# Kernel tuning notes

Hardware: AMD Instinct MI355X
Metric: run time of the kernel (lower is better)

## Reference

```python
import jax, jax.numpy as jnp
import numpy as np

B, S, D, H = 64, 2048, 512, 512


def setup_inputs() -> dict:
    key = jax.random.key(0)
    ks = jax.random.split(key, 8)
    return {
        "hidden": jax.random.normal(ks[0], (B, D), dtype=jnp.float32),
        "context": jax.random.normal(ks[1], (B, S, D), dtype=jnp.float32),
        "mask": jax.random.randint(ks[2], (B, S), 0, 2).astype(bool),
        "Wd": jax.random.normal(ks[3], (H, D), dtype=jnp.float32) * 0.05,
        "bd": jax.random.normal(ks[4], (H,), dtype=jnp.float32) * 0.05,
        "We": jax.random.normal(ks[5], (H, D), dtype=jnp.float32) * 0.05,
        "be": jax.random.normal(ks[6], (H,), dtype=jnp.float32) * 0.05,
        "V": jax.random.normal(ks[7], (H,), dtype=jnp.float32) * 0.05,
    }


def reference(hidden, context, mask, Wd, bd, We, be, V):
    # di = d_linear(hidden): [B, H]
    di = hidden @ Wd.T + bd
    # ei = e_linear(context): [B, S, H]
    ei = jnp.einsum("bsd,hd->bsh", context, We) + be
    # additive score u_i = V . tanh(di + ei): [B, S]
    ui = jnp.einsum("h,bsh->bs", V, jnp.tanh(di[:, None, :] + ei))
    # masked positions get -inf (ui[mask] = -inf)
    ui = jnp.where(mask, -jnp.inf, ui)
    alpha = jax.nn.softmax(ui, axis=-1)  # [B, S]
    # context aggregation uses the PROJECTED context ei (as in torch code)
    attention_hidden_state = jnp.einsum("bsh,bs->bh", ei, alpha)
    return alpha, attention_hidden_state
```

## Files before the change

### kernel.cpp

```cpp
#include <hip/hip_runtime.h>
#include <cstdint>

#define B_ 64
#define S_ 2048
#define D_ 512
#define H_ 512

using f32x4  = __attribute__((ext_vector_type(4))) float;
using bf16x8 = __attribute__((ext_vector_type(8))) short;

__device__ __forceinline__ unsigned short f2bf(float f) {
  unsigned u = __float_as_uint(f);
  u += 0x7FFFu + ((u >> 16) & 1u);
  return (unsigned short)(u >> 16);
}
__device__ __forceinline__ float bf2f(unsigned short h) {
  return __uint_as_float(((unsigned)h) << 16);
}
__device__ __forceinline__ float fast_tanh(float x) {
  float t = __builtin_amdgcn_exp2f(x * 2.8853900817779268f);
  return 1.0f - 2.0f * __builtin_amdgcn_rcpf(t + 1.0f);
}

__device__ __forceinline__ void gl_lds16(const unsigned short* g, unsigned short* l) {
  __builtin_amdgcn_global_load_lds(
      (const __attribute__((address_space(1))) unsigned int*)g,
      (__attribute__((address_space(3))) unsigned int*)l, 16, 0, 0);
}

__global__ void k_cvt(const float* __restrict__ src, unsigned short* __restrict__ dst, int n8) {
  int i = blockIdx.x * 256 + threadIdx.x;
  if (i >= n8) return;
  const f32x4* p = (const f32x4*)(src + (size_t)i * 8);
  f32x4 a = p[0], b = p[1];
  bf16x8 o;
  o[0] = (short)f2bf(a[0]); o[1] = (short)f2bf(a[1]);
  o[2] = (short)f2bf(a[2]); o[3] = (short)f2bf(a[3]);
  o[4] = (short)f2bf(b[0]); o[5] = (short)f2bf(b[1]);
  o[6] = (short)f2bf(b[2]); o[7] = (short)f2bf(b[3]);
  *(bf16x8*)(dst + (size_t)i * 8) = o;
}

__global__ void k_di(const float* __restrict__ hidden, const float* __restrict__ Wd,
                     const float* __restrict__ bd, float* __restrict__ di) {
  int idx = blockIdx.x * 256 + threadIdx.x;
  int h = idx >> 6;
  int b = idx & 63;
  const f32x4* hp = (const f32x4*)(hidden + (size_t)b * D_);
  const f32x4* wp = (const f32x4*)(Wd + (size_t)h * D_);
  float acc = 0.f;
#pragma unroll 8
  for (int i = 0; i < D_ / 4; ++i) {
    f32x4 x = hp[i], y = wp[i];
    acc += x[0] * y[0] + x[1] * y[1] + x[2] * y[2] + x[3] * y[3];
  }
  di[b * H_ + h] = acc + bd[h];
}

__global__ __launch_bounds__(256, 4) void k_ei_gemm(
    const unsigned short* __restrict__ A, const unsigned short* __restrict__ Bw,
    const float* __restrict__ be, const float* __restrict__ V,
    const float* __restrict__ di, float* __restrict__ ui4) {
  __shared__ __align__(16) unsigned short ldsA[2][128 * 32];
  __shared__ __align__(16) unsigned short ldsB[2][128 * 32];
  __shared__ float ured[4][64];

  const int bid = blockIdx.x;
  const int swz = (bid & 7) * 512 + (bid >> 3);
  const int row0 = (swz >> 2) << 7;
  const int nt   = swz & 3;
  const int col0 = nt << 7;

  const int t  = threadIdx.x;
  const int l  = t & 63;
  const int w  = t >> 6;
  const int wm = (w >> 1) << 6;
  const int wn = (w & 1) << 6;
  const int lr = l & 15;
  const int lg = l >> 4;

  const int sr = l >> 2;
  const int sc = ((l & 3) ^ ((sr >> 1) & 3)) << 3;
  const unsigned short* gA = A + (size_t)(row0 + w * 32 + sr) * D_ + sc;
  const unsigned short* gB = Bw + (size_t)(col0 + w * 32 + sr) * D_ + sc;
  unsigned short* lA[2] = {&ldsA[0][w * 1024], &ldsA[1][w * 1024]};
  unsigned short* lB[2] = {&ldsB[0][w * 1024], &ldsB[1][w * 1024]};

  const int rslot = (lg ^ ((lr >> 1) & 3)) << 3;

#define STAGE(bf, kk) do {                      \
    const int k0_ = (kk) << 5;                  \
    gl_lds16(gA + k0_,           lA[bf]);       \
    gl_lds16(gA + 16 * D_ + k0_, lA[bf] + 512); \
    gl_lds16(gB + k0_,           lB[bf]);       \
    gl_lds16(gB + 16 * D_ + k0_, lB[bf] + 512); \
  } while (0)

  f32x4 acc[4][4];
  const f32x4 z = {0.f, 0.f, 0.f, 0.f};
#pragma unroll
  for (int mi = 0; mi < 4; ++mi)
#pragma unroll
    for (int ni = 0; ni < 4; ++ni) acc[mi][ni] = z;

  STAGE(0, 0);
  int cur = 0;
  for (int kt = 0; kt < 16; ++kt) {
    __syncthreads();
    if (kt < 15) STAGE(cur ^ 1, kt + 1);

    bf16x8 af[4], bq[4];
#pragma unroll
    for (int mi = 0; mi < 4; ++mi)
      af[mi] = *(const bf16x8*)&ldsA[cur][(wm + mi * 16 + lr) * 32 + rslot];
#pragma unroll
    for (int ni = 0; ni < 4; ++ni)
      bq[ni] = *(const bf16x8*)&ldsB[cur][(wn + ni * 16 + lr) * 32 + rslot];
#pragma unroll
    for (int mi = 0; mi < 4; ++mi)
#pragma unroll
      for (int ni = 0; ni < 4; ++ni)
        acc[mi][ni] = __builtin_amdgcn_mfma_f32_16x16x32_bf16(
            af[mi], bq[ni], acc[mi][ni], 0, 0, 0);
    cur ^= 1;
  }
#undef STAGE

  const int b = row0 >> 11;
  float uacc[4][4];
#pragma unroll
  for (int mi = 0; mi < 4; ++mi)
#pragma unroll
    for (int j = 0; j < 4; ++j) uacc[mi][j] = 0.f;

#pragma unroll
  for (int ni = 0; ni < 4; ++ni) {
    const int gc = col0 + wn + ni * 16 + lr;
    const float vv = V[gc];
    const float base = di[b * H_ + gc] + be[gc];
#pragma unroll
    for (int mi = 0; mi < 4; ++mi)
#pragma unroll
      for (int j = 0; j < 4; ++j)
        uacc[mi][j] += vv * fast_tanh(base + acc[mi][ni][j]);
  }
#pragma unroll
  for (int mi = 0; mi < 4; ++mi)
#pragma unroll
    for (int j = 0; j < 4; ++j) {
      float s = uacc[mi][j];
      s += __shfl_xor(s, 1);
      s += __shfl_xor(s, 2);
      s += __shfl_xor(s, 4);
      s += __shfl_xor(s, 8);
      if (lr == 0) ured[w][mi * 16 + (lg << 2) + j] = s;
    }
  __syncthreads();
  if (t < 128) {
    const int r = t & 63, half = t >> 6;
    const float v = ured[half * 2][r] + ured[half * 2 + 1][r];
    ui4[nt * (B_ * S_) + row0 + half * 64 + r] = v;
  }
}

__global__ void k_softmax(const float* __restrict__ ui4, const void* __restrict__ mask,
                          float* __restrict__ alpha) {
  __shared__ float red[4];
  __shared__ int sfl;
  const int b = blockIdx.x, t = threadIdx.x;
  const int l = t & 63, w = t >> 6;

  if (t == 0) sfl = 0;
  const unsigned int* mw = (const unsigned int*)mask;
  unsigned det = (mw[b * 512 + t] | mw[b * 512 + 256 + t]) & 0xFFFFFF00u;
  __syncthreads();
  if (det) atomicOr(&sfl, 1);
  __syncthreads();
  const int fl = sfl;

  float u[8];
#pragma unroll
  for (int i = 0; i < 8; ++i) {
    const int idx = b * S_ + t + i * 256;
    const int msk = fl ? (int)((const unsigned char*)mask)[idx]
                       : ((const int*)mask)[idx];
    const float uv = ui4[idx] + ui4[idx + B_ * S_] + ui4[idx + 2 * B_ * S_] +
                     ui4[idx + 3 * B_ * S_];
    u[i] = msk ? -__builtin_inff() : uv;
  }

  float mx = u[0];
#pragma unroll
  for (int i = 1; i < 8; ++i) mx = fmaxf(mx, u[i]);
#pragma unroll
  for (int off = 32; off; off >>= 1) mx = fmaxf(mx, __shfl_xor(mx, off));
  if (l == 0) red[w] = mx;
  __syncthreads();
  mx = fmaxf(fmaxf(red[0], red[1]), fmaxf(red[2], red[3]));
  __syncthreads();

  float p[8];
  float s = 0.f;
#pragma unroll
  for (int i = 0; i < 8; ++i) {
    p[i] = __builtin_amdgcn_exp2f((u[i] - mx) * 1.4426950408889634f);
    s += p[i];
  }
#pragma unroll
  for (int off = 32; off; off >>= 1) s += __shfl_xor(s, off);
  if (l == 0) red[w] = s;
  __syncthreads();
  s = red[0] + red[1] + red[2] + red[3];

  const float inv = 1.0f / s;
#pragma unroll
  for (int i = 0; i < 8; ++i) alpha[b * S_ + t + i * 256] = p[i] * inv;
}

__global__ void k_wsum(const unsigned short* __restrict__ ctxb, const float* __restrict__ alpha,
                       float* __restrict__ part) {
  __shared__ float red[3][512];
  const int b = blockIdx.x >> 4, chunk = blockIdx.x & 15;
  const int t = threadIdx.x;
  const int h0 = (t & 63) << 3;
  const int sw = t >> 6;
  const int s0 = chunk << 7;

  float acc[8] = {0.f, 0.f, 0.f, 0.f, 0.f, 0.f, 0.f, 0.f};
#pragma unroll 4
  for (int k = 0; k < 32; ++k) {
    const int s = s0 + sw + (k << 2);
    const float a = alpha[b * S_ + s];
    bf16x8 e = *(const bf16x8*)(ctxb + ((size_t)(b * S_ + s)) * D_ + h0);
#pragma unroll
    for (int j = 0; j < 8; ++j) acc[j] += a * bf2f((unsigned short)e[j]);
  }
  if (sw) {
#pragma unroll
    for (int j = 0; j < 8; ++j) red[sw - 1][h0 + j] = acc[j];
  }
  __syncthreads();
  if (sw == 0) {
#pragma unroll
    for (int j = 0; j < 8; ++j)
      part[((chunk << 6) + b) * 512 + h0 + j] =
          acc[j] + red[0][h0 + j] + red[1][h0 + j] + red[2][h0 + j];
  }
}

__global__ void k_collapse(const float* __restrict__ part, float* __restrict__ wsum) {
  const int i = blockIdx.x * 256 + threadIdx.x;
  const int b = i >> 9, d = i & 511;
  float s = 0.f;
#pragma unroll
  for (int c = 0; c < 16; ++c) s += part[((c << 6) + b) * 512 + d];
  wsum[i] = s;
}

__global__ void k_out1(const float* __restrict__ wsum, const float* __restrict__ We,
                       const float* __restrict__ be, float* __restrict__ out1) {
  int idx = blockIdx.x * 256 + threadIdx.x;
  int h = idx >> 6;
  int b = idx & 63;
  const f32x4* wp = (const f32x4*)(wsum + (size_t)b * D_);
  const f32x4* ep = (const f32x4*)(We + (size_t)h * D_);
  float acc = 0.f;
#pragma unroll 8
  for (int i = 0; i < D_ / 4; ++i) {
    f32x4 x = wp[i], y = ep[i];
    acc += x[0] * y[0] + x[1] * y[1] + x[2] * y[2] + x[3] * y[3];
  }
  out1[b * H_ + h] = acc + be[h];
}

extern "C" void kernel_launch(void* const* d_in, const int* in_sizes, int n_in,
                              void* d_out, int out_size, void* d_ws, size_t ws_size,
                              hipStream_t stream) {
  const float* hidden = (const float*)d_in[0];
  const float* ctx    = (const float*)d_in[1];
  const void*  mask   = d_in[2];
  const float* Wd     = (const float*)d_in[3];
  const float* bd     = (const float*)d_in[4];
  const float* We     = (const float*)d_in[5];
  const float* be     = (const float*)d_in[6];
  const float* V      = (const float*)d_in[7];

  float* out   = (float*)d_out;
  float* alpha = out;
  float* out1  = out + B_ * S_;

  char* ws = (char*)d_ws;
  const size_t off_ctxb = 0;
  const size_t off_u2   = off_ctxb + (size_t)B_ * S_ * D_ * 2;
  const size_t off_r3   = off_u2 + 4ull * B_ * S_ * 4;
  const size_t off_web  = off_r3 + (size_t)B_ * H_ * 4;

  unsigned short* ctxb = (unsigned short*)(ws + off_ctxb);
  float* ui4  = (float*)(ws + off_u2);
  float* part = (float*)(ws + off_u2);
  float* di   = (float*)(ws + off_r3);
  float* wsum = (float*)(ws + off_r3);
  unsigned short* Web = (unsigned short*)(ws + off_web);

  k_cvt<<<(B_ * S_ * D_ / 8) / 256, 256, 0, stream>>>(ctx, ctxb, B_ * S_ * D_ / 8);
  k_cvt<<<(H_ * D_ / 8) / 256, 256, 0, stream>>>(We, Web, H_ * D_ / 8);
  k_di<<<(B_ * H_) / 256, 256, 0, stream>>>(hidden, Wd, bd, di);
  k_ei_gemm<<<(B_ * S_ / 128) * 4, 256, 0, stream>>>(ctxb, Web, be, V, di, ui4);
  k_softmax<<<B_, 256, 0, stream>>>(ui4, mask, alpha);
  k_wsum<<<B_ * 16, 256, 0, stream>>>(ctxb, alpha, part);
  k_collapse<<<(B_ * D_) / 256, 256, 0, stream>>>(part, wsum);
  k_out1<<<(B_ * H_) / 256, 256, 0, stream>>>(wsum, We, be, out1);
}
```

Baseline: 246.8 us.

## Enlarge ei GEMM tile to 256x128 with 8 waves and explicit vmcnt pipelining

The ei GEMM block now covers 256 rows by 128 columns using 512 threads (8 waves), so each B tile loaded into LDS is reused across twice as many rows. The main loop preloads two stages up front and replaces __syncthreads with raw s_barrier plus explicit vmcnt waits, so direct-to-LDS loads can stay in flight across iterations. It also raises wave priority around the MFMA block. The hand-written vmcnt counts and raw barriers depend on exact load ordering and could give races if the compiler emits other memory ops, and the larger block raises LDS use per block, which may reduce occupancy.

```diff
diff --git a/kernel.cpp b/kernel.cpp
--- a/kernel.cpp
+++ b/kernel.cpp
@@ -26,6 +26,12 @@
   __builtin_amdgcn_global_load_lds(
       (const __attribute__((address_space(1))) unsigned int*)g,
       (__attribute__((address_space(3))) unsigned int*)l, 16, 0, 0);
+}
+
+__device__ __forceinline__ void barrier_raw() {
+  asm volatile("" ::: "memory");
+  __builtin_amdgcn_s_barrier();
+  asm volatile("" ::: "memory");
 }
 
 __global__ void k_cvt(const float* __restrict__ src, unsigned short* __restrict__ dst, int n8) {
@@ -57,17 +63,17 @@
   di[b * H_ + h] = acc + bd[h];
 }
 
-__global__ __launch_bounds__(256, 4) void k_ei_gemm(
+__global__ __launch_bounds__(512, 4) void k_ei_gemm(
     const unsigned short* __restrict__ A, const unsigned short* __restrict__ Bw,
     const float* __restrict__ be, const float* __restrict__ V,
     const float* __restrict__ di, float* __restrict__ ui4) {
-  __shared__ __align__(16) unsigned short ldsA[2][128 * 32];
+  __shared__ __align__(16) unsigned short ldsA[2][256 * 32];
   __shared__ __align__(16) unsigned short ldsB[2][128 * 32];
-  __shared__ float ured[4][64];
+  __shared__ float ured[8][64];
 
   const int bid = blockIdx.x;
-  const int swz = (bid & 7) * 512 + (bid >> 3);
-  const int row0 = (swz >> 2) << 7;
+  const int swz = (bid & 7) * 256 + (bid >> 3);
+  const int row0 = (swz >> 2) << 8;
   const int nt   = swz & 3;
   const int col0 = nt << 7;
 
@@ -80,20 +86,17 @@
   const int lg = l >> 4;
 
   const int sr = l >> 2;
-  const int sc = ((l & 3) ^ ((sr >> 1) & 3)) << 3;
-  const unsigned short* gA = A + (size_t)(row0 + w * 32 + sr) * D_ + sc;
-  const unsigned short* gB = Bw + (size_t)(col0 + w * 32 + sr) * D_ + sc;
-  unsigned short* lA[2] = {&ldsA[0][w * 1024], &ldsA[1][w * 1024]};
-  unsigned short* lB[2] = {&ldsB[0][w * 1024], &ldsB[1][w * 1024]};
+  const int sc = ((l & 3) ^ ((l >> 3) & 3)) << 3;
+  const unsigned short* gA = A + (size_t)(row0 + w * 16 + sr) * D_ + sc;
+  const unsigned short* gB = Bw + (size_t)(col0 + w * 16 + sr) * D_ + sc;
 
   const int rslot = (lg ^ ((lr >> 1) & 3)) << 3;
 
-#define STAGE(bf, kk) do {                      \
-    const int k0_ = (kk) << 5;                  \
-    gl_lds16(gA + k0_,           lA[bf]);       \
-    gl_lds16(gA + 16 * D_ + k0_, lA[bf] + 512); \
-    gl_lds16(gB + k0_,           lB[bf]);       \
-    gl_lds16(gB + 16 * D_ + k0_, lB[bf] + 512); \
+#define STAGE(bf, kk) do {                                          \
+    const int k0_ = (kk) << 5;                                      \
+    gl_lds16(gA + k0_,            &ldsA[bf][w * 512]);              \
+    gl_lds16(gA + 128 * D_ + k0_, &ldsA[bf][4096 + w * 512]);       \
+    gl_lds16(gB + k0_,            &ldsB[bf][w * 512]);              \
   } while (0)
 
   f32x4 acc[4][4];
@@ -104,25 +107,35 @@
     for (int ni = 0; ni < 4; ++ni) acc[mi][ni] = z;
 
   STAGE(0, 0);
-  int cur = 0;
+  STAGE(1, 1);
+
   for (int kt = 0; kt < 16; ++kt) {
-    __syncthreads();
-    if (kt < 15) STAGE(cur ^ 1, kt + 1);
-
+    if (kt < 15)
+      asm volatile("s_waitcnt vmcnt(3)" ::: "memory");
+    else
+      asm volatile("s_waitcnt vmcnt(0)" ::: "memory");
+    barrier_raw();
+
+    const int bf = kt & 1;
     bf16x8 af[4], bq[4];
 #pragma unroll
     for (int mi = 0; mi < 4; ++mi)
-      af[mi] = *(const bf16x8*)&ldsA[cur][(wm + mi * 16 + lr) * 32 + rslot];
+      af[mi] = *(const bf16x8*)&ldsA[bf][(wm + mi * 16 + lr) * 32 + rslot];
 #pragma unroll
     for (int ni = 0; ni < 4; ++ni)
-      bq[ni] = *(const bf16x8*)&ldsB[cur][(wn + ni * 16 + lr) * 32 + rslot];
+      bq[ni] = *(const bf16x8*)&ldsB[bf][(wn + ni * 16 + lr) * 32 + rslot];
+
+    __builtin_amdgcn_s_setprio(1);
 #pragma unroll
     for (int mi = 0; mi < 4; ++mi)
 #pragma unroll
       for (int ni = 0; ni < 4; ++ni)
         acc[mi][ni] = __builtin_amdgcn_mfma_f32_16x16x32_bf16(
             af[mi], bq[ni], acc[mi][ni], 0, 0, 0);
-    cur ^= 1;
+    __builtin_amdgcn_s_setprio(0);
+
+    barrier_raw();
+    if (kt + 2 < 16) STAGE(bf, kt + 2);
   }
 #undef STAGE
 
@@ -156,10 +169,9 @@
       if (lr == 0) ured[w][mi * 16 + (lg << 2) + j] = s;
     }
   __syncthreads();
-  if (t < 128) {
-    const int r = t & 63, half = t >> 6;
-    const float v = ured[half * 2][r] + ured[half * 2 + 1][r];
-    ui4[nt * (B_ * S_) + row0 + half * 64 + r] = v;
+  if (t < 256) {
+    const int band = t >> 6, r = t & 63;
+    ui4[nt * (B_ * S_) + row0 + t] = ured[band * 2][r] + ured[band * 2 + 1][r];
   }
 }
 
@@ -305,7 +317,7 @@
   k_cvt<<<(B_ * S_ * D_ / 8) / 256, 256, 0, stream>>>(ctx, ctxb, B_ * S_ * D_ / 8);
   k_cvt<<<(H_ * D_ / 8) / 256, 256, 0, stream>>>(We, Web, H_ * D_ / 8);
   k_di<<<(B_ * H_) / 256, 256, 0, stream>>>(hidden, Wd, bd, di);
-  k_ei_gemm<<<(B_ * S_ / 128) * 4, 256, 0, stream>>>(ctxb, Web, be, V, di, ui4);
+  k_ei_gemm<<<(B_ * S_ / 256) * 4, 512, 0, stream>>>(ctxb, Web, be, V, di, ui4);
   k_softmax<<<B_, 256, 0, stream>>>(ui4, mask, alpha);
   k_wsum<<<B_ * 16, 256, 0, stream>>>(ctxb, alpha, part);
   k_collapse<<<(B_ * D_) / 256, 256, 0, stream>>>(part, wsum);
```

Result: faster. 239.0 us (-3.2%).

## Fuse bf16 context conversion into GEMM register staging and merge small kernels

Applied to the files above, without the earlier changes.

The separate full-context fp32-to-bf16 conversion pass is removed. The GEMM now loads fp32 context tiles into registers, converts them with packed cvt instructions and writes them to swizzled LDS, using register-prefetch double buffering, raw barriers and setprio around the MFMA block. The di and We-conversion kernels are merged into one prep launch, and collapse plus out1 are merged into one tail kernel. k_wsum now reads fp32 context directly, which doubles that kernel's read traffic but avoids writing and rereading a bf16 copy; occupancy bounds drop from 4 to 3.

```diff
diff --git a/kernel.cpp b/kernel.cpp
--- a/kernel.cpp
+++ b/kernel.cpp
@@ -8,57 +8,60 @@
 
 using f32x4  = __attribute__((ext_vector_type(4))) float;
 using bf16x8 = __attribute__((ext_vector_type(8))) short;
+using u32x2  = __attribute__((ext_vector_type(2))) unsigned int;
 
 __device__ __forceinline__ unsigned short f2bf(float f) {
   unsigned u = __float_as_uint(f);
   u += 0x7FFFu + ((u >> 16) & 1u);
   return (unsigned short)(u >> 16);
 }
-__device__ __forceinline__ float bf2f(unsigned short h) {
-  return __uint_as_float(((unsigned)h) << 16);
+__device__ __forceinline__ unsigned int cvtpk(float lo, float hi) {
+  unsigned int r;
+  asm("v_cvt_pk_bf16_f32 %0, %1, %2" : "=v"(r) : "v"(lo), "v"(hi));
+  return r;
 }
 __device__ __forceinline__ float fast_tanh(float x) {
   float t = __builtin_amdgcn_exp2f(x * 2.8853900817779268f);
   return 1.0f - 2.0f * __builtin_amdgcn_rcpf(t + 1.0f);
 }
 
-__device__ __forceinline__ void gl_lds16(const unsigned short* g, unsigned short* l) {
-  __builtin_amdgcn_global_load_lds(
-      (const __attribute__((address_space(1))) unsigned int*)g,
-      (__attribute__((address_space(3))) unsigned int*)l, 16, 0, 0);
-}
-
-__global__ void k_cvt(const float* __restrict__ src, unsigned short* __restrict__ dst, int n8) {
-  int i = blockIdx.x * 256 + threadIdx.x;
-  if (i >= n8) return;
-  const f32x4* p = (const f32x4*)(src + (size_t)i * 8);
-  f32x4 a = p[0], b = p[1];
-  bf16x8 o;
-  o[0] = (short)f2bf(a[0]); o[1] = (short)f2bf(a[1]);
-  o[2] = (short)f2bf(a[2]); o[3] = (short)f2bf(a[3]);
-  o[4] = (short)f2bf(b[0]); o[5] = (short)f2bf(b[1]);
-  o[6] = (short)f2bf(b[2]); o[7] = (short)f2bf(b[3]);
-  *(bf16x8*)(dst + (size_t)i * 8) = o;
-}
-
-__global__ void k_di(const float* __restrict__ hidden, const float* __restrict__ Wd,
-                     const float* __restrict__ bd, float* __restrict__ di) {
-  int idx = blockIdx.x * 256 + threadIdx.x;
-  int h = idx >> 6;
-  int b = idx & 63;
-  const f32x4* hp = (const f32x4*)(hidden + (size_t)b * D_);
-  const f32x4* wp = (const f32x4*)(Wd + (size_t)h * D_);
-  float acc = 0.f;
+__device__ __forceinline__ void barrier_raw() {
+  asm volatile("" ::: "memory");
+  __builtin_amdgcn_s_barrier();
+  asm volatile("" ::: "memory");
+}
+
+__global__ void k_prep(const float* __restrict__ hidden, const float* __restrict__ Wd,
+                       const float* __restrict__ bd, float* __restrict__ di,
+                       const float* __restrict__ We, unsigned short* __restrict__ Web) {
+  if (blockIdx.x < 128) {
+    int idx = blockIdx.x * 256 + threadIdx.x;
+    int h = idx >> 6;
+    int b = idx & 63;
+    const f32x4* hp = (const f32x4*)(hidden + (size_t)b * D_);
+    const f32x4* wp = (const f32x4*)(Wd + (size_t)h * D_);
+    float acc = 0.f;
 #pragma unroll 8
-  for (int i = 0; i < D_ / 4; ++i) {
-    f32x4 x = hp[i], y = wp[i];
-    acc += x[0] * y[0] + x[1] * y[1] + x[2] * y[2] + x[3] * y[3];
-  }
-  di[b * H_ + h] = acc + bd[h];
-}
-
-__global__ __launch_bounds__(256, 4) void k_ei_gemm(
-    const unsigned short* __restrict__ A, const unsigned short* __restrict__ Bw,
+    for (int i = 0; i < D_ / 4; ++i) {
+      f32x4 x = hp[i], y = wp[i];
+      acc += x[0] * y[0] + x[1] * y[1] + x[2] * y[2] + x[3] * y[3];
+    }
+    di[b * H_ + h] = acc + bd[h];
+  } else {
+    int i = (blockIdx.x - 128) * 256 + threadIdx.x;
+    const f32x4* p = (const f32x4*)(We + (size_t)i * 8);
+    f32x4 a = p[0], b = p[1];
+    bf16x8 o;
+    o[0] = (short)f2bf(a[0]); o[1] = (short)f2bf(a[1]);
+    o[2] = (short)f2bf(a[2]); o[3] = (short)f2bf(a[3]);
+    o[4] = (short)f2bf(b[0]); o[5] = (short)f2bf(b[1]);
+    o[6] = (short)f2bf(b[2]); o[7] = (short)f2bf(b[3]);
+    *(bf16x8*)(Web + (size_t)i * 8) = o;
+  }
+}
+
+__global__ __launch_bounds__(256, 3) void k_ei_gemm(
+    const float* __restrict__ A, const unsigned short* __restrict__ Bw,
     const float* __restrict__ be, const float* __restrict__ V,
     const float* __restrict__ di, float* __restrict__ ui4) {
   __shared__ __align__(16) unsigned short ldsA[2][128 * 32];
@@ -79,21 +82,41 @@
   const int lr = l & 15;
   const int lg = l >> 4;
 
-  const int sr = l >> 2;
-  const int sc = ((l & 3) ^ ((sr >> 1) & 3)) << 3;
-  const unsigned short* gA = A + (size_t)(row0 + w * 32 + sr) * D_ + sc;
-  const unsigned short* gB = Bw + (size_t)(col0 + w * 32 + sr) * D_ + sc;
-  unsigned short* lA[2] = {&ldsA[0][w * 1024], &ldsA[1][w * 1024]};
-  unsigned short* lB[2] = {&ldsB[0][w * 1024], &ldsB[1][w * 1024]};
-
-  const int rslot = (lg ^ ((lr >> 1) & 3)) << 3;
-
-#define STAGE(bf, kk) do {                      \
-    const int k0_ = (kk) << 5;                  \
-    gl_lds16(gA + k0_,           lA[bf]);       \
-    gl_lds16(gA + 16 * D_ + k0_, lA[bf] + 512); \
-    gl_lds16(gB + k0_,           lB[bf]);       \
-    gl_lds16(gB + 16 * D_ + k0_, lB[bf] + 512); \
+  const float* gA = A + (size_t)(row0 + w * 32 + (l >> 3)) * D_ + ((l & 7) << 2);
+  const unsigned short* gB = Bw + (size_t)(col0 + w * 32 + (l >> 2)) * D_ + ((l & 3) << 3);
+
+  const int sA = (((l & 7) >> 1) ^ ((l >> 4) & 3));
+  const int eA0 = (w * 32 + (l >> 3)) * 32 + sA * 8 + (l & 1) * 4;
+  const int sB = ((l & 3) ^ ((l >> 3) & 3));
+  const int eB0 = (w * 32 + (l >> 2)) * 32 + sB * 8;
+
+  const int rs = (lg ^ ((lr >> 1) & 3)) << 3;
+
+  f32x4  rA0, rA1, rA2, rA3;
+  bf16x8 rB0, rB1;
+
+#define LOAD(kk) do {                                   \
+    const float* a_ = gA + ((kk) << 5);                 \
+    rA0 = *(const f32x4*)(a_);                          \
+    rA1 = *(const f32x4*)(a_ + 8 * D_);                 \
+    rA2 = *(const f32x4*)(a_ + 16 * D_);                \
+    rA3 = *(const f32x4*)(a_ + 24 * D_);                \
+    const unsigned short* b_ = gB + ((kk) << 5);        \
+    rB0 = *(const bf16x8*)(b_);                         \
+    rB1 = *(const bf16x8*)(b_ + 16 * D_);               \
+  } while (0)
+
+#define WRITE(bf) do {                                                  \
+    u32x2 p0 = {cvtpk(rA0[0], rA0[1]), cvtpk(rA0[2], rA0[3])};          \
+    u32x2 p1 = {cvtpk(rA1[0], rA1[1]), cvtpk(rA1[2], rA1[3])};          \
+    u32x2 p2 = {cvtpk(rA2[0], rA2[1]), cvtpk(rA2[2], rA2[3])};          \
+    u32x2 p3 = {cvtpk(rA3[0], rA3[1]), cvtpk(rA3[2], rA3[3])};          \
+    *(u32x2*)&ldsA[bf][eA0]       = p0;                                 \
+    *(u32x2*)&ldsA[bf][eA0 + 256] = p1;                                 \
+    *(u32x2*)&ldsA[bf][eA0 + 512] = p2;                                 \
+    *(u32x2*)&ldsA[bf][eA0 + 768] = p3;                                 \
+    *(bf16x8*)&ldsB[bf][eB0]       = rB0;                               \
+    *(bf16x8*)&ldsB[bf][eB0 + 512] = rB1;                               \
   } while (0)
 
   f32x4 acc[4][4];
@@ -103,28 +126,37 @@
 #pragma unroll
     for (int ni = 0; ni < 4; ++ni) acc[mi][ni] = z;
 
-  STAGE(0, 0);
-  int cur = 0;
+  LOAD(0);
+  WRITE(0);
+  LOAD(1);
+
   for (int kt = 0; kt < 16; ++kt) {
-    __syncthreads();
-    if (kt < 15) STAGE(cur ^ 1, kt + 1);
+    const int bf = kt & 1;
+    asm volatile("s_waitcnt lgkmcnt(0)" ::: "memory");
+    barrier_raw();
 
     bf16x8 af[4], bq[4];
 #pragma unroll
     for (int mi = 0; mi < 4; ++mi)
-      af[mi] = *(const bf16x8*)&ldsA[cur][(wm + mi * 16 + lr) * 32 + rslot];
+      af[mi] = *(const bf16x8*)&ldsA[bf][(wm + mi * 16 + lr) * 32 + rs];
 #pragma unroll
     for (int ni = 0; ni < 4; ++ni)
-      bq[ni] = *(const bf16x8*)&ldsB[cur][(wn + ni * 16 + lr) * 32 + rslot];
+      bq[ni] = *(const bf16x8*)&ldsB[bf][(wn + ni * 16 + lr) * 32 + rs];
+
+    if (kt + 1 < 16) WRITE(bf ^ 1);
+    if (kt + 2 < 16) LOAD(kt + 2);
+
+    __builtin_amdgcn_s_setprio(1);
 #pragma unroll
     for (int mi = 0; mi < 4; ++mi)
 #pragma unroll
       for (int ni = 0; ni < 4; ++ni)
         acc[mi][ni] = __builtin_amdgcn_mfma_f32_16x16x32_bf16(
             af[mi], bq[ni], acc[mi][ni], 0, 0, 0);
-    cur ^= 1;
-  }
-#undef STAGE
+    __builtin_amdgcn_s_setprio(0);
+  }
+#undef LOAD
+#undef WRITE
 
   const int b = row0 >> 11;
   float uacc[4][4];
@@ -158,8 +190,8 @@
   __syncthreads();
   if (t < 128) {
     const int r = t & 63, half = t >> 6;
-    const float v = ured[half * 2][r] + ured[half * 2 + 1][r];
-    ui4[nt * (B_ * S_) + row0 + half * 64 + r] = v;
+    ui4[nt * (B_ * S_) + row0 + half * 64 + r] =
+        ured[half * 2][r] + ured[half * 2 + 1][r];
   }
 }
 
@@ -217,7 +249,7 @@
   for (int i = 0; i < 8; ++i) alpha[b * S_ + t + i * 256] = p[i] * inv;
 }
 
-__global__ void k_wsum(const unsigned short* __restrict__ ctxb, const float* __restrict__ alpha,
+__global__ void k_wsum(const float* __restrict__ ctx, const float* __restrict__ alpha,
                        float* __restrict__ part) {
   __shared__ float red[3][512];
   const int b = blockIdx.x >> 4, chunk = blockIdx.x & 15;
@@ -227,13 +259,16 @@
   const int s0 = chunk << 7;
 
   float acc[8] = {0.f, 0.f, 0.f, 0.f, 0.f, 0.f, 0.f, 0.f};
-#pragma unroll 4
+#pragma unroll 2
   for (int k = 0; k < 32; ++k) {
     const int s = s0 + sw + (k << 2);
     const float a = alpha[b * S_ + s];
-    bf16x8 e = *(const bf16x8*)(ctxb + ((size_t)(b * S_ + s)) * D_ + h0);
-#pragma unroll
-    for (int j = 0; j < 8; ++j) acc[j] += a * bf2f((unsigned short)e[j]);
+    const f32x4* e = (const f32x4*)(ctx + ((size_t)(b * S_ + s)) * D_ + h0);
+    f32x4 e0 = e[0], e1 = e[1];
+#pragma unroll
+    for (int j = 0; j < 4; ++j) acc[j] += a * e0[j];
+#pragma unroll
+    for (int j = 0; j < 4; ++j) acc[4 + j] += a * e1[j];
   }
   if (sw) {
 #pragma unroll
@@ -248,29 +283,26 @@
   }
 }
 
-__global__ void k_collapse(const float* __restrict__ part, float* __restrict__ wsum) {
-  const int i = blockIdx.x * 256 + threadIdx.x;
-  const int b = i >> 9, d = i & 511;
+__global__ void k_tail(const float* __restrict__ part, const float* __restrict__ We,
+                       const float* __restrict__ be, float* __restrict__ out1) {
+  __shared__ float wsum_s[512];
+  const int b = blockIdx.x, t = threadIdx.x;
+
   float s = 0.f;
 #pragma unroll
-  for (int c = 0; c < 16; ++c) s += part[((c << 6) + b) * 512 + d];
-  wsum[i] = s;
-}
-
-__global__ void k_out1(const float* __restrict__ wsum, const float* __restrict__ We,
-                       const float* __restrict__ be, float* __restrict__ out1) {
-  int idx = blockIdx.x * 256 + threadIdx.x;
-  int h = idx >> 6;
-  int b = idx & 63;
-  const f32x4* wp = (const f32x4*)(wsum + (size_t)b * D_);
-  const f32x4* ep = (const f32x4*)(We + (size_t)h * D_);
+  for (int c = 0; c < 16; ++c) s += part[((c << 6) + b) * 512 + t];
+  wsum_s[t] = s;
+  __syncthreads();
+
+  const f32x4* wp = (const f32x4*)wsum_s;
+  const f32x4* ep = (const f32x4*)(We + (size_t)t * D_);
   float acc = 0.f;
 #pragma unroll 8
   for (int i = 0; i < D_ / 4; ++i) {
     f32x4 x = wp[i], y = ep[i];
     acc += x[0] * y[0] + x[1] * y[1] + x[2] * y[2] + x[3] * y[3];
   }
-  out1[b * H_ + h] = acc + be[h];
+  out1[b * H_ + t] = acc + be[t];
 }
 
 extern "C" void kernel_launch(void* const* d_in, const int* in_sizes, int n_in,
@@ -290,24 +322,18 @@
   float* out1  = out + B_ * S_;
 
   char* ws = (char*)d_ws;
-  const size_t off_ctxb = 0;
-  const size_t off_u2   = off_ctxb + (size_t)B_ * S_ * D_ * 2;
-  const size_t off_r3   = off_u2 + 4ull * B_ * S_ * 4;
-  const size_t off_web  = off_r3 + (size_t)B_ * H_ * 4;
-
-  unsigned short* ctxb = (unsigned short*)(ws + off_ctxb);
+  const size_t off_u2  = 0;
+  const size_t off_r3  = off_u2 + 4ull * B_ * S_ * 4;
+  const size_t off_web = off_r3 + (size_t)B_ * H_ * 4;
+
   float* ui4  = (float*)(ws + off_u2);
   float* part = (float*)(ws + off_u2);
   float* di   = (float*)(ws + off_r3);
-  float* wsum = (float*)(ws + off_r3);
   unsigned short* Web = (unsigned short*)(ws + off_web);
 
-  k_cvt<<<(B_ * S_ * D_ / 8) / 256, 256, 0, stream>>>(ctx, ctxb, B_ * S_ * D_ / 8);
-  k_cvt<<<(H_ * D_ / 8) / 256, 256, 0, stream>>>(We, Web, H_ * D_ / 8);
-  k_di<<<(B_ * H_) / 256, 256, 0, stream>>>(hidden, Wd, bd, di);
-  k_ei_gemm<<<(B_ * S_ / 128) * 4, 256, 0, stream>>>(ctxb, Web, be, V, di, ui4);
+  k_prep<<<256, 256, 0, stream>>>(hidden, Wd, bd, di, We, Web);
+  k_ei_gemm<<<(B_ * S_ / 128) * 4, 256, 0, stream>>>(ctx, Web, be, V, di, ui4);
   k_softmax<<<B_, 256, 0, stream>>>(ui4, mask, alpha);
-  k_wsum<<<B_ * 16, 256, 0, stream>>>(ctxb, alpha, part);
-  k_collapse<<<(B_ * D_) / 256, 256, 0, stream>>>(part, wsum);
-  k_out1<<<(B_ * H_) / 256, 256, 0, stream>>>(wsum, We, be, out1);
-}
+  k_wsum<<<B_ * 16, 256, 0, stream>>>(ctx, alpha, part);
+  k_tail<<<B_, 512, 0, stream>>>(part, We, be, out1);
+}
```

Result: faster. 208.3 us (-15.6%).
